# Optimization experiments

Measured on AMD Instinct MI355X. Metric: run time of the kernel, lower is better.

Reference implementation:

```python
import jax, jax.numpy as jnp
import numpy as np
import math

H = 128
HEADS = 2
NEG = -float(1 << 32)
BN_EPS = 1e-5
LN_EPS = 1e-5


def _bn_eval(x, g, b):
    # BatchNorm1d in eval mode with running_mean=0, running_var=1
    return g * (x / jnp.sqrt(1.0 + BN_EPS)) + b


def _ln(x, g, b):
    mu = x.mean(-1, keepdims=True)
    var = ((x - mu) ** 2).mean(-1, keepdims=True)
    return g * (x - mu) / jnp.sqrt(var + LN_EPS) + b


def _multi_embed(tables, idx):
    # tables [F,V,H], idx [N,F] -> sum_f tables[f, idx[:,f]]  (ogb Atom/BondEncoder)
    F = tables.shape[0]
    return tables[jnp.arange(F)[None, :], idx].sum(axis=1)


def _gin_graph(x, edge_attr, edge_index, batch, num_graphs, atom_emb, bond_emb, eps, w1, b1, g1, be1, w2, b2, g2, be2):
    h = _multi_embed(atom_emb, x)  # [N,H]
    tgt, src = edge_index[0], edge_index[1]
    L = eps.shape[0]
    for l in range(L):
        e = _multi_embed(bond_emb[l], edge_attr)  # [E,H]
        msg = jax.nn.relu(h[src] + e)
        agg = jax.ops.segment_sum(msg, tgt, num_segments=h.shape[0])
        z = (1.0 + eps[l]) * h + agg
        z = jax.nn.relu(_bn_eval(z @ w1[l] + b1[l], g1[l], be1[l])) @ w2[l] + b2[l]
        h = _bn_eval(z, g2[l], be2[l])
        if l != L - 1:
            h = jax.nn.relu(h)  # dropout is identity in eval mode
    s = jax.ops.segment_sum(h, batch, num_segments=num_graphs)
    c = jax.ops.segment_sum(jnp.ones_like(h), batch, num_segments=num_graphs)
    return s / (c + 1e-9)  # mean pooling per graph


def _sab(X, wq, bq, wk, bk, wv, bv, wo, bo, l1g, l1b, l2g, l2b):
    # MAB(X, X) with HEADS heads, use_ln=True. X: [B,S,H]
    B, S, _ = X.shape
    dh = H // HEADS

    def split(T):  # torch split(last)+cat(dim0): head-major [HEADS*B, S, dh]
        return T.reshape(B, S, HEADS, dh).transpose(2, 0, 1, 3).reshape(HEADS * B, S, dh)

    Qs, Ks, Vs = split(X @ wq + bq), split(X @ wk + bk), split(X @ wv + bv)
    A = jax.nn.softmax(jnp.einsum('bqd,bkd->bqk', Qs, Ks) / math.sqrt(dh), axis=-1)
    O = Qs + jnp.einsum('bqk,bkd->bqd', A, Vs)
    O = O.reshape(HEADS, B, S, dh).transpose(1, 2, 0, 3).reshape(B, S, H)
    O = _ln(O, l1g, l1b)
    O = _ln(O @ wo + bo, l2g, l2b)
    return O


def setup_inputs() -> dict:
    key = jax.random.key(0)
    ks = iter(jax.random.split(key, 64))
    nk = lambda: next(ks)
    V, L = 64, 4
    NS, ES = 60000, 140000
    NM, EM = 150000, 350000
    S, M, D, B = 492, 600, 200, 64
    f32 = jnp.float32
    w = lambda *shp: jax.random.normal(nk(), shp, f32) * 0.05
    inp = {}
    inp['atom_emb'] = w(2, 9, V, H)
    inp['bond_emb'] = w(2, L, 3, V, H)
    inp['gin_eps'] = jnp.zeros((2, L), f32)
    inp['gin_w1'] = w(2, L, H, 2 * H); inp['gin_b1'] = jnp.zeros((2, L, 2 * H), f32)
    inp['gin_bn1_g'] = jnp.ones((2, L, 2 * H), f32); inp['gin_bn1_b'] = jnp.zeros((2, L, 2 * H), f32)
    inp['gin_w2'] = w(2, L, 2 * H, H); inp['gin_b2'] = jnp.zeros((2, L, H), f32)
    inp['gin_bn2_g'] = jnp.ones((2, L, H), f32); inp['gin_bn2_b'] = jnp.zeros((2, L, H), f32)
    for nm in ['sab_wq', 'sab_wk', 'sab_wv', 'sab_wo']:
        inp[nm] = w(H, H)
    for nm in ['sab_bq', 'sab_bk', 'sab_bv', 'sab_bo', 'sab_ln1_b', 'sab_ln2_b']:
        inp[nm] = jnp.zeros((H,), f32)
    inp['sab_ln1_g'] = jnp.ones((H,), f32); inp['sab_ln2_g'] = jnp.ones((H,), f32)
    inp['agg_wq'] = w(H, H); inp['agg_bq'] = jnp.zeros((H,), f32)
    inp['agg_wk'] = w(H, H); inp['agg_bk'] = jnp.zeros((H,), f32)
    inp['score_w1'] = w(H, H // 2); inp['score_b1'] = jnp.zeros((H // 2,), f32)
    inp['score_w2'] = w(H // 2, 1); inp['score_b2'] = jnp.zeros((1,), f32)
    inp['patient_emb'] = jax.random.uniform(nk(), (B, S), f32)
    inp['average_projection'] = jax.random.uniform(nk(), (D, M), f32) / M
    inp['sub_x'] = jax.random.randint(nk(), (NS, 9), 0, V)
    inp['sub_edge_attr'] = jax.random.randint(nk(), (ES, 3), 0, V)
    inp['sub_edge_index'] = jax.random.randint(nk(), (2, ES), 0, NS)
    inp['sub_batch'] = jax.random.randint(nk(), (NS,), 0, S)
    inp['mol_x'] = jax.random.randint(nk(), (NM, 9), 0, V)
    inp['mol_edge_attr'] = jax.random.randint(nk(), (EM, 3), 0, V)
    inp['mol_edge_index'] = jax.random.randint(nk(), (2, EM), 0, NM)
    inp['mol_batch'] = jax.random.randint(nk(), (NM,), 0, M)
    mask = jax.random.bernoulli(nk(), 0.3, (D, S))
    inp['mask'] = mask.at[:, 0].set(False)
    inp['num_sub'] = S
    inp['num_mol'] = M
    return inp


def reference(atom_emb, bond_emb, gin_eps, gin_w1, gin_b1, gin_bn1_g, gin_bn1_b, gin_w2, gin_b2, gin_bn2_g, gin_bn2_b, sab_wq, sab_bq, sab_wk, sab_bk, sab_wv, sab_bv, sab_wo, sab_bo, sab_ln1_g, sab_ln1_b, sab_ln2_g, sab_ln2_b, agg_wq, agg_bq, agg_wk, agg_bk, score_w1, score_b1, score_w2, score_b2, patient_emb, average_projection, sub_x, sub_edge_attr, sub_edge_index, sub_batch, mol_x, mol_edge_attr, mol_edge_index, mol_batch, mask, num_sub, num_mol):
    # substructure encoder (GINGraph #0) + SAB interaction
    sub = _gin_graph(sub_x, sub_edge_attr, sub_edge_index, sub_batch, num_sub, atom_emb[0], bond_emb[0], gin_eps[0], gin_w1[0], gin_b1[0], gin_bn1_g[0], gin_bn1_b[0], gin_w2[0], gin_b2[0], gin_bn2_g[0], gin_bn2_b[0])
    sub = _sab(sub[None], sab_wq, sab_bq, sab_wk, sab_bk, sab_wv, sab_bv, sab_wo, sab_bo, sab_ln1_g, sab_ln1_b, sab_ln2_g, sab_ln2_b)[0]  # [S,H]
    # molecule encoder (GINGraph #1) + drug-level averaging
    mol = _gin_graph(mol_x, mol_edge_attr, mol_edge_index, mol_batch, num_mol, atom_emb[1], bond_emb[1], gin_eps[1], gin_w1[1], gin_b1[1], gin_bn1_g[1], gin_bn1_b[1], gin_w2[1], gin_b2[1], gin_bn2_g[1], gin_bn2_b[1])
    mol_emb = average_projection @ mol  # [D,H]
    # AttnAgg: masked attention, per-patient reweighting via diag(fix_feat)
    Q = mol_emb @ agg_wq + agg_bq
    K = sub @ agg_wk + agg_bk
    attn = (Q @ K.T) / math.sqrt(H)
    attn = jax.nn.softmax(jnp.where(mask, NEG, attn), axis=-1)  # [D,S]
    agg = jnp.einsum('ds,bs,sh->bdh', attn, patient_emb, sub)  # [B,D,H]
    logits = (jax.nn.relu(agg @ score_w1 + score_b1) @ score_w2 + score_b2)[..., 0]
    return jax.nn.sigmoid(logits)  # y_prob [B,D]
```

## Files before the change

### kernel.cpp

```cpp
#include <hip/hip_runtime.h>


typedef short short8 __attribute__((ext_vector_type(8)));
typedef unsigned short us8 __attribute__((ext_vector_type(8)));
typedef float f32x4 __attribute__((ext_vector_type(4)));
typedef unsigned short us4 __attribute__((ext_vector_type(4)));
typedef unsigned int u32;

#define BN_RSQ 0.9999950000374997f
#define LN_EPS 1e-5f
#define NEGBIG -4294967296.0f

__device__ __forceinline__ unsigned short f2bf(float x) {
  union { float f; unsigned int u; } v; v.f = x;
  unsigned int r = v.u + 0x7fffu + ((v.u >> 16) & 1u);
  return (unsigned short)(r >> 16);
}
__device__ __forceinline__ float bf2f(unsigned short x) {
  union { unsigned int u; float f; } v; v.u = ((unsigned int)x) << 16;
  return v.f;
}

__global__ __launch_bounds__(256) void prep_all(
    const float* __restrict__ w1, const float* __restrict__ w2,
    unsigned short* __restrict__ w1t, unsigned short* __restrict__ w2t,
    const float* __restrict__ bond, unsigned short* __restrict__ bt16, int bonde,
    const unsigned char* __restrict__ m, int* __restrict__ flags, int maskn) {
  __shared__ int lf[2];
  int b = blockIdx.x;
  if (b < 1024) {
    int i = b * 256 + threadIdx.x;
    int gl = i >> 15;
    int k1 = (i >> 8) & 127, c1 = i & 255;
    w1t[(gl << 15) + c1 * 128 + k1] = f2bf(w1[i]);
    int k2 = (i >> 7) & 255, c2 = i & 127;
    w2t[(gl << 15) + c2 * 256 + k2] = f2bf(w2[i]);
    return;
  }
  if (b < 1792) {
    int i = (b - 1024) * 256 + threadIdx.x;
    if (i < bonde) bt16[i] = f2bf(bond[i]);
    return;
  }
  if (threadIdx.x == 0) { lf[0] = 0; lf[1] = 0; }
  __syncthreads();
  int f0 = 0, f1 = 0;
  for (int i = (b - 1792) * 256 + threadIdx.x; i < maskn; i += 64 * 256) {
    if (m[i]) { if ((i & 3) == 0) f0 = 1; else f1 = 1; }
  }
  if (f0) atomicOr(&lf[0], 1);
  if (f1) atomicOr(&lf[1], 1);
  __syncthreads();
  if (threadIdx.x == 0) {
    if (lf[0]) atomicOr(flags, 1);
    if (lf[1]) atomicOr(flags + 1, 1);
  }
}

__global__ void build_count(const int* __restrict__ ei_m, int Em,
                            const int* __restrict__ ei_s, int Es,
                            const int* __restrict__ bm, int Nm,
                            const int* __restrict__ bs, int Ns,
                            int* __restrict__ deg_e, int* __restrict__ deg_n,
                            int M, int NmR) {
  int i = blockIdx.x * 256 + threadIdx.x;
  if (i < Em) { atomicAdd(&deg_e[ei_m[i]], 1); return; }
  i -= Em;
  if (i < Es) { atomicAdd(&deg_e[NmR + ei_s[i]], 1); return; }
  i -= Es;
  if (i < Nm) { atomicAdd(&deg_n[bm[i]], 1); return; }
  i -= Nm;
  if (i < Ns) { atomicAdd(&deg_n[M + bs[i]], 1); }
}

__global__ __launch_bounds__(256) void scan_block2(
    const int* __restrict__ cntE, int nE, int* __restrict__ exclE, int* __restrict__ bsumE, int nbE,
    const int* __restrict__ cntN, int nN, int* __restrict__ exclN, int* __restrict__ bsumN) {
  const int* cnt; int n; int* excl; int* bsum; int blk;
  if (blockIdx.x < (unsigned)nbE) { cnt = cntE; n = nE; excl = exclE; bsum = bsumE; blk = blockIdx.x; }
  else { cnt = cntN; n = nN; excl = exclN; bsum = bsumN; blk = blockIdx.x - nbE; }
  int gid = blk * 256 + threadIdx.x;
  int lane = threadIdx.x & 63, w = threadIdx.x >> 6;
  int v = (gid < n) ? cnt[gid] : 0;
  int x = v;
#pragma unroll
  for (int off = 1; off < 64; off <<= 1) {
    int y = __shfl_up(x, off, 64);
    if (lane >= off) x += y;
  }
  __shared__ int wt[4];
  if (lane == 63) wt[w] = x;
  __syncthreads();
  int add = 0;
  for (int i = 0; i < w; i++) add += wt[i];
  x += add;
  if (gid < n) excl[gid] = x - v;
  if (threadIdx.x == 255) bsum[blk] = x;
}

__global__ __launch_bounds__(1024) void scan_top2(int* __restrict__ bsumE, int nE,
                                                  int* __restrict__ bsumN, int nN) {
  int* bsum = blockIdx.x ? bsumN : bsumE;
  int n = blockIdx.x ? nN : nE;
  int t = threadIdx.x;
  int lane = t & 63, w = t >> 6;
  int v = (t < n) ? bsum[t] : 0;
  int x = v;
#pragma unroll
  for (int off = 1; off < 64; off <<= 1) {
    int y = __shfl_up(x, off, 64);
    if (lane >= off) x += y;
  }
  __shared__ int wt[16];
  if (lane == 63) wt[w] = x;
  __syncthreads();
  int add = 0;
  for (int i = 0; i < w; i++) add += wt[i];
  x += add;
  if (t < n) bsum[t] = x - v;
}

__global__ void finalize2(const int* __restrict__ exclE, const int* __restrict__ bsumE,
                          int nE, int totE, int* __restrict__ rowE,
                          const int* __restrict__ exclN, const int* __restrict__ bsumN,
                          int nN, int totN, int* __restrict__ rowN) {
  int i = blockIdx.x * 256 + threadIdx.x;
  if (i <= nE) {
    rowE[i] = (i < nE) ? (exclE[i] + bsumE[i >> 8]) : totE;
    return;
  }
  int j = i - nE - 1;
  if (j <= nN) rowN[j] = (j < nN) ? (exclN[j] + bsumN[j >> 8]) : totN;
}

__global__ void scatter2(const int* __restrict__ ei_m, const int* __restrict__ ea_m, int Em,
                         const int* __restrict__ ei_s, const int* __restrict__ ea_s, int Es, int NmR,
                         const int* __restrict__ rowptr_e, int* __restrict__ cur_e,
                         int4* __restrict__ epool,
                         const int* __restrict__ bm, int Nm,
                         const int* __restrict__ bs, int Ns, int M,
                         const int* __restrict__ rowptr_n, int* __restrict__ cur_n,
                         int* __restrict__ npool) {
  int i = blockIdx.x * 256 + threadIdx.x;
  if (i < Em + Es) {
    int g, src, a0, a1, a2;
    if (i < Em) {
      g = ei_m[i]; src = ei_m[Em + i];
      a0 = ea_m[i * 3]; a1 = ea_m[i * 3 + 1]; a2 = ea_m[i * 3 + 2];
    } else {
      int j = i - Em;
      g = NmR + ei_s[j]; src = NmR + ei_s[Es + j];
      a0 = ea_s[j * 3]; a1 = ea_s[j * 3 + 1]; a2 = ea_s[j * 3 + 2];
    }
    int slot = rowptr_e[g] + atomicAdd(&cur_e[g], 1);
    int p0 = a0 * 128, p1 = (64 + a1) * 128, p2 = (128 + a2) * 128;
    epool[slot] = make_int4(src * 128, 0, p0 | (p1 << 16), p2);
    return;
  }
  int k = i - (Em + Es);
  if (k >= Nm + Ns) return;
  int g, node;
  if (k < Nm) { g = bm[k]; node = k; }
  else { int j = k - Nm; g = M + bs[j]; node = NmR + j; }
  int slot = rowptr_n[g] + atomicAdd(&cur_n[g], 1);
  npool[slot] = node;
}

__global__ void embed2(const int* __restrict__ xm, const int* __restrict__ xs,
                       const float* __restrict__ atab, int Nm, int Ns, int NmR,
                       unsigned short* __restrict__ h) {
  int i = blockIdx.x * 256 + threadIdx.x;
  const int* x; const float* table; int n, c, outn;
  if (i < Nm * 128) {
    n = i >> 7; c = i & 127; x = xm; table = atab + (size_t)9 * 64 * 128; outn = n;
  } else {
    int j = i - Nm * 128;
    if (j >= Ns * 128) return;
    n = j >> 7; c = j & 127; x = xs; table = atab; outn = NmR + n;
  }
  float s = 0.f;
#pragma unroll
  for (int f = 0; f < 9; f++) {
    int v = x[n * 9 + f];
    s += table[(f * 64 + v) * 128 + c];
  }
  h[(size_t)outn * 128 + c] = f2bf(s);
}

__global__ __launch_bounds__(256, 4) void gin_fused3(
    const unsigned short* __restrict__ hin, unsigned short* __restrict__ hout,
    const float* __restrict__ eps_all, int l, int NmR,
    const unsigned short* __restrict__ bt16,
    const int4* __restrict__ epool, const int* __restrict__ rowptr_e,
    const unsigned short* __restrict__ w1t_a, const float* __restrict__ b1_a,
    const float* __restrict__ g1_a, const float* __restrict__ be1_a,
    const unsigned short* __restrict__ w2t_a, const float* __restrict__ b2_a,
    const float* __restrict__ g2_a, const float* __restrict__ be2_a) {
  __shared__ __align__(16) unsigned char smem[38144];
  unsigned short* z1s = (unsigned short*)smem;
  unsigned short* zs  = (unsigned short*)(smem + 20736);
  int t = threadIdx.x;
  int r0 = blockIdx.x * 64;
  int g = (r0 < NmR) ? 1 : 0;
  int gl = g * 4 + l;
  const unsigned short* bt = bt16 + (size_t)gl * 3 * 64 * 128;
  const unsigned short* w1t = w1t_a + (size_t)gl * 32768;
  const unsigned short* w2t = w2t_a + (size_t)gl * 32768;
  const float* b1 = b1_a + gl * 256;
  const float* g1 = g1_a + gl * 256;
  const float* be1 = be1_a + gl * 256;
  const float* b2 = b2_a + gl * 128;
  const float* g2 = g2_a + gl * 128;
  const float* be2 = be2_a + gl * 128;
  float eps1 = 1.0f + eps_all[gl];
  int do_relu = (l != 3);

#pragma unroll
  for (int p = 0; p < 2; p++) {
    int lr = p * 32 + (t >> 3);
    int n = r0 + lr;
    int cb = (t & 7) * 16;
    float lo[8], hi[8];
    {
      const u32* hr = (const u32*)(hin + (size_t)n * 128 + cb);
      uint4 h0v = *(const uint4*)hr;
      uint4 h1v = *(const uint4*)(hr + 4);
      u32 hd[8] = {h0v.x, h0v.y, h0v.z, h0v.w, h1v.x, h1v.y, h1v.z, h1v.w};
#pragma unroll
      for (int j = 0; j < 8; j++) {
        lo[j] = eps1 * __uint_as_float(hd[j] << 16);
        hi[j] = eps1 * __uint_as_float(hd[j] & 0xffff0000u);
      }
    }
    int e0 = rowptr_e[n], e1 = rowptr_e[n + 1];
    for (int e = e0; e < e1; e++) {
      int4 rec = epool[e];
      const u32* hs = (const u32*)(hin + rec.x + cb);
      const u32* q0 = (const u32*)(bt + (rec.z & 0xffff) + cb);
      const u32* q1 = (const u32*)(bt + (((unsigned)rec.z) >> 16) + cb);
      const u32* q2 = (const u32*)(bt + rec.w + cb);
      uint4 A0 = *(const uint4*)hs, A1 = *(const uint4*)(hs + 4);
      uint4 B0 = *(const uint4*)q0, B1 = *(const uint4*)(q0 + 4);
      uint4 C0 = *(const uint4*)q1, C1 = *(const uint4*)(q1 + 4);
      uint4 D0 = *(const uint4*)q2, D1 = *(const uint4*)(q2 + 4);
      u32 ad[8] = {A0.x, A0.y, A0.z, A0.w, A1.x, A1.y, A1.z, A1.w};
      u32 bd[8] = {B0.x, B0.y, B0.z, B0.w, B1.x, B1.y, B1.z, B1.w};
      u32 cd[8] = {C0.x, C0.y, C0.z, C0.w, C1.x, C1.y, C1.z, C1.w};
      u32 dd[8] = {D0.x, D0.y, D0.z, D0.w, D1.x, D1.y, D1.z, D1.w};
#pragma unroll
      for (int j = 0; j < 8; j++) {
        float sl = __uint_as_float(ad[j] << 16) + __uint_as_float(bd[j] << 16)
                 + __uint_as_float(cd[j] << 16) + __uint_as_float(dd[j] << 16);
        float sh = __uint_as_float(ad[j] & 0xffff0000u) + __uint_as_float(bd[j] & 0xffff0000u)
                 + __uint_as_float(cd[j] & 0xffff0000u) + __uint_as_float(dd[j] & 0xffff0000u);
        lo[j] += fmaxf(sl, 0.f);
        hi[j] += fmaxf(sh, 0.f);
      }
    }
    u32 od[8];
#pragma unroll
    for (int j = 0; j < 8; j++)
      od[j] = (u32)f2bf(lo[j]) | (((u32)f2bf(hi[j])) << 16);
    u32* zr = (u32*)(zs + lr * 136 + cb);
    *(uint4*)zr = make_uint4(od[0], od[1], od[2], od[3]);
    *(uint4*)(zr + 4) = make_uint4(od[4], od[5], od[6], od[7]);
  }
  __syncthreads();

  int lane = t & 63, wave = t >> 6;
  int quad = lane >> 4, l16 = lane & 15;
  {
    short8 bw[4][4];
    int cb = wave * 64;
#pragma unroll
    for (int nt = 0; nt < 4; nt++) {
      const unsigned short* p = w1t + (cb + nt * 16 + l16) * 128 + quad * 8;
#pragma unroll
      for (int kc = 0; kc < 4; kc++) bw[nt][kc] = *(const short8*)(p + kc * 32);
    }
    for (int mt = 0; mt < 4; mt++) {
      short8 af[4];
      const unsigned short* zrow = zs + (mt * 16 + l16) * 136 + quad * 8;
#pragma unroll
      for (int kc = 0; kc < 4; kc++)
        af[kc] = *(const short8*)(zrow + kc * 32);
#pragma unroll
      for (int nt = 0; nt < 4; nt++) {
        f32x4 acc = {0.f, 0.f, 0.f, 0.f};
#pragma unroll
        for (int kc = 0; kc < 4; kc++)
          acc = __builtin_amdgcn_mfma_f32_16x16x32_bf16(af[kc], bw[nt][kc], acc, 0, 0, 0);
        int c = cb + nt * 16 + l16;
        float sc = g1[c] * BN_RSQ, sh = be1[c], bb = b1[c];
#pragma unroll
        for (int reg = 0; reg < 4; reg++) {
          int r = mt * 16 + quad * 4 + reg;
          float y = (acc[reg] + bb) * sc + sh;
          z1s[r * 264 + c] = f2bf(fmaxf(y, 0.f));
        }
      }
      __syncthreads();
    }
  }
  {
    short8 bw[2][8];
    int cb = wave * 32;
#pragma unroll
    for (int nt = 0; nt < 2; nt++) {
      const unsigned short* p = w2t + (cb + nt * 16 + l16) * 256 + quad * 8;
#pragma unroll
      for (int kc = 0; kc < 8; kc++) bw[nt][kc] = *(const short8*)(p + kc * 32);
    }
    for (int mt = 0; mt < 4; mt++) {
      short8 af[8];
      const unsigned short* zrow = z1s + (mt * 16 + l16) * 264 + quad * 8;
#pragma unroll
      for (int kc = 0; kc < 8; kc++)
        af[kc] = *(const short8*)(zrow + kc * 32);
      __syncthreads();
#pragma unroll
      for (int nt = 0; nt < 2; nt++) {
        f32x4 acc = {0.f, 0.f, 0.f, 0.f};
#pragma unroll
        for (int kc = 0; kc < 8; kc++)
          acc = __builtin_amdgcn_mfma_f32_16x16x32_bf16(af[kc], bw[nt][kc], acc, 0, 0, 0);
        int c = cb + nt * 16 + l16;
        float sc = g2[c] * BN_RSQ, sh = be2[c], bb = b2[c];
#pragma unroll
        for (int reg = 0; reg < 4; reg++) {
          int r = mt * 16 + quad * 4 + reg;
          float y = (acc[reg] + bb) * sc + sh;
          if (do_relu) y = fmaxf(y, 0.f);
          z1s[r * 264 + c] = f2bf(y);
        }
      }
    }
  }
  __syncthreads();
  for (int i = t; i < 1024; i += 256) {
    int r = i >> 4, c8 = (i & 15) * 8;
    us8 v = *(const us8*)(z1s + r * 264 + c8);
    *(us8*)(hout + (size_t)(r0 + r) * 128 + c8) = v;
  }
}

__global__ __launch_bounds__(128) void pool_csr(const unsigned short* __restrict__ h,
                                                const int* __restrict__ npool,
                                                const int* __restrict__ rowptr_n,
                                                float* __restrict__ pooled, int nseg) {
  int m = blockIdx.x;
  if (m >= nseg) return;
  int st = rowptr_n[m];
  int e = rowptr_n[m + 1];
  int len = e - st;
  int c = threadIdx.x;
  float s = 0.f;
  int i = st;
  for (; i + 3 < e; i += 4) {
    int n0 = npool[i], n1 = npool[i + 1], n2 = npool[i + 2], n3 = npool[i + 3];
    float v0 = bf2f(h[(size_t)n0 * 128 + c]);
    float v1 = bf2f(h[(size_t)n1 * 128 + c]);
    float v2 = bf2f(h[(size_t)n2 * 128 + c]);
    float v3 = bf2f(h[(size_t)n3 * 128 + c]);
    s += (v0 + v1) + (v2 + v3);
  }
  for (; i < e; i++) s += bf2f(h[(size_t)npool[i] * 128 + c]);
  pooled[m * 128 + c] = s / ((float)len + 1e-9f);
}

__global__ __launch_bounds__(256) void gemm_tile(const float* __restrict__ A, const float* __restrict__ W,
                                                 const float* __restrict__ bias, float* __restrict__ C,
                                                 int K) {
  __shared__ float As[608];
  __shared__ float red[128];
  int r = blockIdx.x;
  int t = threadIdx.x;
  for (int i = t; i < K; i += 256) As[i] = A[(size_t)r * K + i];
  __syncthreads();
  int c = t & 127, half = t >> 7;
  int Kh = K >> 1;
  int k0 = half * Kh, k1 = k0 + Kh;
  float acc = 0.f;
#pragma unroll 8
  for (int k = k0; k < k1; k++) acc = fmaf(As[k], W[(size_t)k * 128 + c], acc);
  if (half) red[c] = acc;
  __syncthreads();
  if (!half) {
    float v = acc + red[c] + (bias ? bias[c] : 0.f);
    C[(size_t)r * 128 + c] = v;
  }
}

__global__ __launch_bounds__(256) void gemm_qkv(const float* __restrict__ A,
                                                const float* __restrict__ W0, const float* __restrict__ bi0, float* __restrict__ C0,
                                                const float* __restrict__ W1, const float* __restrict__ bi1, float* __restrict__ C1,
                                                const float* __restrict__ W2, const float* __restrict__ bi2, float* __restrict__ C2) {
  __shared__ float As[128];
  __shared__ float red[128];
  int r = blockIdx.x, which = blockIdx.y;
  const float* W = (which == 0) ? W0 : (which == 1) ? W1 : W2;
  const float* bias = (which == 0) ? bi0 : (which == 1) ? bi1 : bi2;
  float* C = (which == 0) ? C0 : (which == 1) ? C1 : C2;
  int t = threadIdx.x;
  if (t < 128) As[t] = A[(size_t)r * 128 + t];
  __syncthreads();
  int c = t & 127, half = t >> 7;
  int k0 = half * 64, k1 = k0 + 64;
  float acc = 0.f;
#pragma unroll 8
  for (int k = k0; k < k1; k++) acc = fmaf(As[k], W[(size_t)k * 128 + c], acc);
  if (half) red[c] = acc;
  __syncthreads();
  if (!half) C[(size_t)r * 128 + c] = acc + red[c] + bias[c];
}

__global__ __launch_bounds__(256) void gemm_aggqk(
    const float* __restrict__ Aq, const float* __restrict__ Wq, const float* __restrict__ bq,
    float* __restrict__ Cq, int D,
    const float* __restrict__ Ak, const float* __restrict__ Wk, const float* __restrict__ bk,
    float* __restrict__ Ck) {
  __shared__ float As[128];
  __shared__ float red[128];
  int r = blockIdx.x;
  const float* A; const float* W; const float* bias; float* C; int rr;
  if (r < D) { A = Aq; W = Wq; bias = bq; C = Cq; rr = r; }
  else { A = Ak; W = Wk; bias = bk; C = Ck; rr = r - D; }
  int t = threadIdx.x;
  if (t < 128) As[t] = A[(size_t)rr * 128 + t];
  __syncthreads();
  int c = t & 127, half = t >> 7;
  int k0 = half * 64, k1 = k0 + 64;
  float acc = 0.f;
#pragma unroll 8
  for (int k = k0; k < k1; k++) acc = fmaf(As[k], W[(size_t)k * 128 + c], acc);
  if (half) red[c] = acc;
  __syncthreads();
  if (!half) C[(size_t)rr * 128 + c] = acc + red[c] + bias[c];
}

__global__ __launch_bounds__(256) void gemm_wo_ln(const float* __restrict__ A,
                                                  const float* __restrict__ W, const float* __restrict__ bias,
                                                  const float* __restrict__ lg, const float* __restrict__ lb,
                                                  float* __restrict__ subf) {
  __shared__ float As[128];
  __shared__ float row[128];
  __shared__ float red2[4];
  int r = blockIdx.x;
  int t = threadIdx.x;
  if (t < 128) As[t] = A[(size_t)r * 128 + t];
  __syncthreads();
  int c = t & 127, half = t >> 7;
  int k0 = half * 64, k1 = k0 + 64;
  float acc = 0.f;
#pragma unroll 8
  for (int k = k0; k < k1; k++) acc = fmaf(As[k], W[(size_t)k * 128 + c], acc);
  if (half) row[c] = acc;
  __syncthreads();
  if (!half) row[c] = acc + row[c] + bias[c];
  __syncthreads();
  if (t < 128) {
    float x = row[t];
    float s = x;
    for (int off = 32; off; off >>= 1) s += __shfl_down(s, off);
    if ((t & 63) == 0) red2[t >> 6] = s;
  }
  __syncthreads();
  if (t < 128) {
    float mu = (red2[0] + red2[1]) * (1.f / 128.f);
    float dd = row[t] - mu;
    float v = dd * dd;
    for (int off = 32; off; off >>= 1) v += __shfl_down(v, off);
    if ((t & 63) == 0) red2[2 + (t >> 6)] = v;
  }
  __syncthreads();
  if (t < 128) {
    float mu = (red2[0] + red2[1]) * (1.f / 128.f);
    float var = (red2[2] + red2[3]) * (1.f / 128.f);
    float dd = row[t] - mu;
    subf[(size_t)r * 128 + t] = lg[t] * dd * rsqrtf(var + LN_EPS) + lb[t];
  }
}

__global__ __launch_bounds__(256) void sab_attn(const float* __restrict__ Q, const float* __restrict__ K,
                                                const float* __restrict__ V, float* __restrict__ O, int S) {
  int q = blockIdx.x, hd = blockIdx.y;
  int t = threadIdx.x;
  __shared__ float sc[512];
  __shared__ float red[8];
  __shared__ float pacc[4][64];
  const float* qrow = Q + q * 128 + hd * 64;
  for (int k = t; k < 512; k += 256) {
    float d = -1e30f;
    if (k < S) {
      const float* krow = K + k * 128 + hd * 64;
      d = 0.f;
#pragma unroll
      for (int j = 0; j < 64; j += 4) {
        float4 a = *(const float4*)(qrow + j);
        float4 b = *(const float4*)(krow + j);
        d += a.x * b.x + a.y * b.y + a.z * b.z + a.w * b.w;
      }
      d *= 0.125f;
    }
    sc[k] = d;
  }
  __syncthreads();
  float m = fmaxf(sc[t], sc[t + 256]);
  for (int off = 32; off; off >>= 1) m = fmaxf(m, __shfl_down(m, off));
  if ((t & 63) == 0) red[t >> 6] = m;
  __syncthreads();
  m = fmaxf(fmaxf(red[0], red[1]), fmaxf(red[2], red[3]));
  float p0 = __expf(sc[t] - m), p1 = __expf(sc[t + 256] - m);
  sc[t] = p0; sc[t + 256] = p1;
  float s = p0 + p1;
  for (int off = 32; off; off >>= 1) s += __shfl_down(s, off);
  if ((t & 63) == 0) red[4 + (t >> 6)] = s;
  __syncthreads();
  float inv = 1.f / (red[4] + red[5] + red[6] + red[7]);
  int d = t & 63, part = t >> 6;
  float acc = 0.f;
  for (int k = part; k < S; k += 4) acc += sc[k] * V[k * 128 + hd * 64 + d];
  pacc[part][d] = acc;
  __syncthreads();
  if (part == 0) {
    float o = (pacc[0][d] + pacc[1][d] + pacc[2][d] + pacc[3][d]) * inv;
    O[q * 128 + hd * 64 + d] = qrow[d] + o;
  }
}

__global__ __launch_bounds__(128) void ln_rows(const float* __restrict__ in, float* __restrict__ out,
                                               const float* __restrict__ g, const float* __restrict__ b) {
  int r = blockIdx.x, t = threadIdx.x;
  __shared__ float red[4];
  float x = in[r * 128 + t];
  float s = x;
  for (int off = 32; off; off >>= 1) s += __shfl_down(s, off);
  if ((t & 63) == 0) red[t >> 6] = s;
  __syncthreads();
  float mu = (red[0] + red[1]) * (1.f / 128.f);
  float dd = x - mu;
  float v = dd * dd;
  for (int off = 32; off; off >>= 1) v += __shfl_down(v, off);
  if ((t & 63) == 0) red[2 + (t >> 6)] = v;
  __syncthreads();
  float var = (red[2] + red[3]) * (1.f / 128.f);
  out[r * 128 + t] = g[t] * dd * rsqrtf(var + LN_EPS) + b[t];
}

__global__ __launch_bounds__(256) void agg_attn(const float* __restrict__ Q, const float* __restrict__ Kt,
                                                const void* __restrict__ mask, const int* __restrict__ flags,
                                                float* __restrict__ attn, int D, int S) {
  int d = blockIdx.x, t = threadIdx.x;
  __shared__ float sc[512];
  __shared__ float red[8];
  int layout = (flags[1] == 0) ? 0 : (flags[0] ? 1 : 2);
  const float* qrow = Q + d * 128;
  for (int s = t; s < 512; s += 256) {
    float v = NEGBIG;
    if (s < S) {
      int mi = d * S + s;
      bool msk;
      if (layout == 0)      msk = ((const int*)mask)[mi] != 0;
      else if (layout == 1) msk = ((const unsigned char*)mask)[mi] != 0;
      else                  msk = ((const float*)mask)[mi] != 0.f;
      if (!msk) {
        float dd = 0.f;
        const float* krow = Kt + s * 128;
#pragma unroll
        for (int j = 0; j < 128; j += 4) {
          float4 a = *(const float4*)(qrow + j);
          float4 b = *(const float4*)(krow + j);
          dd += a.x * b.x + a.y * b.y + a.z * b.z + a.w * b.w;
        }
        v = dd * 0.08838834764831845f;
      }
    }
    sc[s] = v;
  }
  __syncthreads();
  float m = fmaxf(sc[t], sc[t + 256]);
  for (int off = 32; off; off >>= 1) m = fmaxf(m, __shfl_down(m, off));
  if ((t & 63) == 0) red[t >> 6] = m;
  __syncthreads();
  m = fmaxf(fmaxf(red[0], red[1]), fmaxf(red[2], red[3]));
  float p0 = __expf(sc[t] - m), p1 = __expf(sc[t + 256] - m);
  float s2 = p0 + p1;
  for (int off = 32; off; off >>= 1) s2 += __shfl_down(s2, off);
  if ((t & 63) == 0) red[4 + (t >> 6)] = s2;
  __syncthreads();
  float inv = 1.f / (red[4] + red[5] + red[6] + red[7]);
  attn[d * S + t] = p0 * inv;
  if (t + 256 < S) attn[d * S + t + 256] = p1 * inv;
}

__global__ void prep_subT(const float* __restrict__ subf, unsigned short* __restrict__ subT, int S) {
  int i = blockIdx.x * 256 + threadIdx.x;
  if (i >= 128 * 512) return;
  int hh = i >> 9, k = i & 511;
  subT[i] = (k < S) ? f2bf(subf[k * 128 + hh]) : (unsigned short)0;
}

__global__ __launch_bounds__(256) void agg_mfma(const float* __restrict__ attn, const float* __restrict__ pat,
                                                const unsigned short* __restrict__ subT,
                                                float* __restrict__ aggT, int D, int S) {
  int d = blockIdx.x, t = threadIdx.x;
  __shared__ unsigned short As[64][40];
  int lane = t & 63, wave = t >> 6;
  int quad = lane >> 4, l16 = lane & 15;
  f32x4 acc[8];
#pragma unroll
  for (int nt = 0; nt < 8; nt++) acc[nt] = (f32x4){0.f, 0.f, 0.f, 0.f};
  const float* arow = attn + d * S;
  int srow = t >> 2, skb = (t & 3) * 8;
  for (int c = 0; c < 16; c++) {
    int s0 = c * 32;
    __syncthreads();
    unsigned short v[8];
#pragma unroll
    for (int j = 0; j < 8; j++) {
      int s = s0 + skb + j;
      float x = (s < S) ? arow[s] * pat[srow * S + s] : 0.f;
      v[j] = f2bf(x);
    }
    *(us4*)&As[srow][skb]     = *(us4*)&v[0];
    *(us4*)&As[srow][skb + 4] = *(us4*)&v[4];
    __syncthreads();
    short8 af = *(const short8*)&As[16 * wave + l16][quad * 8];
#pragma unroll
    for (int nt = 0; nt < 8; nt++) {
      short8 bf = *(const short8*)(subT + (nt * 16 + l16) * 512 + s0 + quad * 8);
      acc[nt] = __builtin_amdgcn_mfma_f32_16x16x32_bf16(af, bf, acc[nt], 0, 0, 0);
    }
  }
#pragma unroll
  for (int nt = 0; nt < 8; nt++) {
    int hh = nt * 16 + l16;
#pragma unroll
    for (int reg = 0; reg < 4; reg++) {
      int b = 16 * wave + quad * 4 + reg;
      aggT[((size_t)(b * D + d)) * 128 + hh] = acc[nt][reg];
    }
  }
}

__global__ __launch_bounds__(256) void score_head(const float* __restrict__ aggT,
                                                  const float* __restrict__ w1, const float* __restrict__ b1,
                                                  const float* __restrict__ w2, const float* __restrict__ b2,
                                                  float* __restrict__ out, int total) {
  int i = blockIdx.x * 4 + (threadIdx.x >> 6);
  int j = threadIdx.x & 63;
  if (i >= total) return;
  const float* av = aggT + (size_t)i * 128;
  float acc = b1[j];
#pragma unroll 8
  for (int k = 0; k < 128; k++) acc = fmaf(av[k], w1[k * 64 + j], acc);
  acc = fmaxf(acc, 0.f) * w2[j];
  for (int off = 32; off; off >>= 1) acc += __shfl_down(acc, off);
  if (j == 0) {
    float x = acc + b2[0];
    out[i] = 1.f / (1.f + __expf(-x));
  }
}

extern "C" void kernel_launch(void* const* d_in, const int* in_sizes, int n_in,
                              void* d_out, int out_size, void* d_ws, size_t ws_size,
                              hipStream_t stream) {
  const float* atom_emb = (const float*)d_in[0];
  const float* bond_emb = (const float*)d_in[1];
  const float* gin_eps  = (const float*)d_in[2];
  const float* gin_w1   = (const float*)d_in[3];
  const float* gin_b1   = (const float*)d_in[4];
  const float* bn1g     = (const float*)d_in[5];
  const float* bn1b     = (const float*)d_in[6];
  const float* gin_w2   = (const float*)d_in[7];
  const float* gin_b2   = (const float*)d_in[8];
  const float* bn2g     = (const float*)d_in[9];
  const float* bn2b     = (const float*)d_in[10];
  const float* sab_wq = (const float*)d_in[11];
  const float* sab_wk = (const float*)d_in[12];
  const float* sab_wv = (const float*)d_in[13];
  const float* sab_wo = (const float*)d_in[14];
  const float* sab_bq = (const float*)d_in[15];
  const float* sab_bk = (const float*)d_in[16];
  const float* sab_bv = (const float*)d_in[17];
  const float* sab_bo = (const float*)d_in[18];
  const float* ln1b = (const float*)d_in[19];
  const float* ln2b = (const float*)d_in[20];
  const float* ln1g = (const float*)d_in[21];
  const float* ln2g = (const float*)d_in[22];
  const float* agg_wq = (const float*)d_in[23];
  const float* agg_bq = (const float*)d_in[24];
  const float* agg_wk = (const float*)d_in[25];
  const float* agg_bk = (const float*)d_in[26];
  const float* score_w1 = (const float*)d_in[27];
  const float* score_b1 = (const float*)d_in[28];
  const float* score_w2 = (const float*)d_in[29];
  const float* score_b2 = (const float*)d_in[30];
  const float* patient  = (const float*)d_in[31];
  const float* avgproj  = (const float*)d_in[32];
  const int* sub_x     = (const int*)d_in[33];
  const int* sub_ea    = (const int*)d_in[34];
  const int* sub_ei    = (const int*)d_in[35];
  const int* sub_batch = (const int*)d_in[36];
  const int* mol_x     = (const int*)d_in[37];
  const int* mol_ea    = (const int*)d_in[38];
  const int* mol_ei    = (const int*)d_in[39];
  const int* mol_batch = (const int*)d_in[40];
  const void* mask     = d_in[41];

  const int Ns = in_sizes[33] / 9, Es = in_sizes[34] / 3;
  const int Nm = in_sizes[37] / 9, Em = in_sizes[38] / 3;
  const int S = 492, M = 600, D = 200, B = 64;
  const int NmR = (Nm + 63) & ~63;
  const int NsR = (Ns + 63) & ~63;
  const int NTOT = NmR + NsR;
  const int NSEG = M + S;
  const int ETOT = Em + Es;
  const int BONDE = 2 * 4 * 3 * 64 * 128;

  char* Wp = (char*)d_ws;
  size_t off = 0;
  auto alloc = [&](size_t bytes) -> void* {
    void* p = Wp + off;
    off = (off + bytes + 255) & ~(size_t)255;
    return p;
  };
  unsigned short* h0 = (unsigned short*)alloc((size_t)NTOT * 128 * 2);
  unsigned short* h1 = (unsigned short*)alloc((size_t)NTOT * 128 * 2);
  unsigned short* w1t = (unsigned short*)alloc(262144 * 2);
  unsigned short* w2t = (unsigned short*)alloc(262144 * 2);
  unsigned short* bt16 = (unsigned short*)alloc((size_t)BONDE * 2);
  int4* epool  = (int4*)alloc((size_t)ETOT * 16);
  int*  npool  = (int*)alloc((size_t)(Nm + Ns) * 4);
  int*  excl_e = (int*)alloc((size_t)NTOT * 4);
  int*  bsum_e = (int*)alloc(1024 * 4);
  int*  excl_n = (int*)alloc((size_t)NSEG * 4);
  int*  bsum_n = (int*)alloc(1024 * 4);
  int*  rowptr_e = (int*)alloc((size_t)(NTOT + 1) * 4);
  int*  rowptr_n = (int*)alloc((size_t)(NSEG + 1) * 4);
  char* zstart = Wp + off;
  int*  deg_e  = (int*)alloc((size_t)NTOT * 4);
  int*  deg_n  = (int*)alloc((size_t)NSEG * 4);
  int*  cur_e  = (int*)alloc((size_t)NTOT * 4);
  int*  cur_n  = (int*)alloc((size_t)NSEG * 4);
  int*  flags  = (int*)alloc(8);
  size_t zsize = (size_t)((Wp + off) - zstart);
  float* pooled_all = (float*)alloc((size_t)NSEG * 128 * 4);
  float* pooled_mol = pooled_all;
  float* pooled_sub = pooled_all + (size_t)M * 128;
  float* Qb   = (float*)alloc((size_t)S * 128 * 4);
  float* Kb   = (float*)alloc((size_t)S * 128 * 4);
  float* Vb   = (float*)alloc((size_t)S * 128 * 4);
  float* Ob   = (float*)alloc((size_t)S * 128 * 4);
  float* subf = (float*)alloc((size_t)S * 128 * 4);
  unsigned short* subT = (unsigned short*)alloc((size_t)128 * 512 * 2);
  float* mol_embb = (float*)alloc((size_t)D * 128 * 4);
  float* aggQb = (float*)alloc((size_t)D * 128 * 4);
  float* aggKb = (float*)alloc((size_t)S * 128 * 4);
  float* attnb = (float*)alloc((size_t)D * S * 4);
  float* aggTb = (float*)alloc((size_t)B * D * 128 * 4);
  (void)ws_size; (void)n_in; (void)out_size;

  hipMemsetAsync(zstart, 0, zsize, stream);
  prep_all<<<1856, 256, 0, stream>>>(gin_w1, gin_w2, w1t, w2t,
                                     bond_emb, bt16, BONDE,
                                     (const unsigned char*)mask, flags, D * S);

  int total_cnt = Em + Es + Nm + Ns;
  build_count<<<(total_cnt + 255) / 256, 256, 0, stream>>>(
      mol_ei, Em, sub_ei, Es, mol_batch, Nm, sub_batch, Ns, deg_e, deg_n, M, NmR);
  int nb_e = (NTOT + 255) / 256;
  int nb_n = (NSEG + 255) / 256;
  scan_block2<<<nb_e + nb_n, 256, 0, stream>>>(deg_e, NTOT, excl_e, bsum_e, nb_e,
                                               deg_n, NSEG, excl_n, bsum_n);
  scan_top2<<<2, 1024, 0, stream>>>(bsum_e, nb_e, bsum_n, nb_n);
  finalize2<<<((NTOT + 1) + (NSEG + 1) + 1 + 255) / 256, 256, 0, stream>>>(
      excl_e, bsum_e, NTOT, ETOT, rowptr_e,
      excl_n, bsum_n, NSEG, Nm + Ns, rowptr_n);
  scatter2<<<(ETOT + Nm + Ns + 255) / 256, 256, 0, stream>>>(
      mol_ei, mol_ea, Em, sub_ei, sub_ea, Es, NmR, rowptr_e, cur_e, epool,
      mol_batch, Nm, sub_batch, Ns, M, rowptr_n, cur_n, npool);

  embed2<<<((Nm + Ns) * 128 + 255) / 256, 256, 0, stream>>>(
      mol_x, sub_x, atom_emb, Nm, Ns, NmR, h0);
  unsigned short* hin = h0; unsigned short* hout = h1;
  for (int l = 0; l < 4; l++) {
    gin_fused3<<<NTOT / 64, 256, 0, stream>>>(
        hin, hout, gin_eps, l, NmR, bt16, epool, rowptr_e,
        w1t, gin_b1, bn1g, bn1b, w2t, gin_b2, bn2g, bn2b);
    unsigned short* tmp = hin; hin = hout; hout = tmp;
  }
  pool_csr<<<NSEG, 128, 0, stream>>>(hin, npool, rowptr_n, pooled_all, NSEG);

  gemm_qkv<<<dim3(S, 3), 256, 0, stream>>>(pooled_sub,
                                           sab_wq, sab_bq, Qb,
                                           sab_wk, sab_bk, Kb,
                                           sab_wv, sab_bv, Vb);
  sab_attn<<<dim3(S, 2), 256, 0, stream>>>(Qb, Kb, Vb, Ob, S);
  ln_rows<<<S, 128, 0, stream>>>(Ob, Ob, ln1g, ln1b);
  gemm_wo_ln<<<S, 256, 0, stream>>>(Ob, sab_wo, sab_bo, ln2g, ln2b, subf);
  prep_subT<<<(128 * 512 + 255) / 256, 256, 0, stream>>>(subf, subT, S);

  gemm_tile<<<D, 256, 0, stream>>>(avgproj, pooled_mol, (const float*)nullptr, mol_embb, 600);

  gemm_aggqk<<<D + S, 256, 0, stream>>>(mol_embb, agg_wq, agg_bq, aggQb, D,
                                        subf, agg_wk, agg_bk, aggKb);
  agg_attn<<<D, 256, 0, stream>>>(aggQb, aggKb, mask, flags, attnb, D, S);
  agg_mfma<<<D, 256, 0, stream>>>(attnb, patient, subT, aggTb, D, S);
  score_head<<<(B * D + 3) / 4, 256, 0, stream>>>(aggTb, score_w1, score_b1, score_w2, score_b2,
                                                  (float*)d_out, B * D);
}
```

Measured before the change: 1.016 ms.

## Compact edge records, stage them in LDS per block, vectorize atom embedding

Shrinks each CSR edge record from 16 to 8 bytes by packing the three bond attribute indices into one 18-bit field and computing table offsets in the kernel. Each GIN block now cooperatively loads its contiguous range of edge records into shared memory (up to a cap, with global fallback beyond it) before the per-node aggregation loop. This replaces the per-thread redundant global reads, since eight threads share each node's records. The atom embedding kernel is also vectorized to four channels per thread with float4 loads and packed bf16 stores. The shared buffer aliases the z1s region, so correctness depends on a barrier before the later writes to z1s.

```diff
diff --git a/kernel.cpp b/kernel.cpp
--- a/kernel.cpp
+++ b/kernel.cpp
@@ -136,7 +136,7 @@
 __global__ void scatter2(const int* __restrict__ ei_m, const int* __restrict__ ea_m, int Em,
                          const int* __restrict__ ei_s, const int* __restrict__ ea_s, int Es, int NmR,
                          const int* __restrict__ rowptr_e, int* __restrict__ cur_e,
-                         int4* __restrict__ epool,
+                         int2* __restrict__ epool,
                          const int* __restrict__ bm, int Nm,
                          const int* __restrict__ bs, int Ns, int M,
                          const int* __restrict__ rowptr_n, int* __restrict__ cur_n,
@@ -153,8 +153,7 @@
       a0 = ea_s[j * 3]; a1 = ea_s[j * 3 + 1]; a2 = ea_s[j * 3 + 2];
     }
     int slot = rowptr_e[g] + atomicAdd(&cur_e[g], 1);
-    int p0 = a0 * 128, p1 = (64 + a1) * 128, p2 = (128 + a2) * 128;
-    epool[slot] = make_int4(src * 128, 0, p0 | (p1 << 16), p2);
+    epool[slot] = make_int2(src * 128, a0 | (a1 << 6) | (a2 << 12));
     return;
   }
   int k = i - (Em + Es);
@@ -170,28 +169,31 @@
                        const float* __restrict__ atab, int Nm, int Ns, int NmR,
                        unsigned short* __restrict__ h) {
   int i = blockIdx.x * 256 + threadIdx.x;
-  const int* x; const float* table; int n, c, outn;
-  if (i < Nm * 128) {
-    n = i >> 7; c = i & 127; x = xm; table = atab + (size_t)9 * 64 * 128; outn = n;
+  const int* x; const float* table; int n, cq, outn;
+  if (i < Nm * 32) {
+    n = i >> 5; cq = (i & 31) * 4; x = xm; table = atab + (size_t)9 * 64 * 128; outn = n;
   } else {
-    int j = i - Nm * 128;
-    if (j >= Ns * 128) return;
-    n = j >> 7; c = j & 127; x = xs; table = atab; outn = NmR + n;
-  }
-  float s = 0.f;
+    int j = i - Nm * 32;
+    if (j >= Ns * 32) return;
+    n = j >> 5; cq = (j & 31) * 4; x = xs; table = atab; outn = NmR + n;
+  }
+  float4 s = make_float4(0.f, 0.f, 0.f, 0.f);
 #pragma unroll
   for (int f = 0; f < 9; f++) {
     int v = x[n * 9 + f];
-    s += table[(f * 64 + v) * 128 + c];
-  }
-  h[(size_t)outn * 128 + c] = f2bf(s);
+    float4 tv = *(const float4*)(table + (size_t)(f * 64 + v) * 128 + cq);
+    s.x += tv.x; s.y += tv.y; s.z += tv.z; s.w += tv.w;
+  }
+  us4 o;
+  o.x = f2bf(s.x); o.y = f2bf(s.y); o.z = f2bf(s.z); o.w = f2bf(s.w);
+  *(us4*)(h + (size_t)outn * 128 + cq) = o;
 }
 
 __global__ __launch_bounds__(256, 4) void gin_fused3(
     const unsigned short* __restrict__ hin, unsigned short* __restrict__ hout,
     const float* __restrict__ eps_all, int l, int NmR,
     const unsigned short* __restrict__ bt16,
-    const int4* __restrict__ epool, const int* __restrict__ rowptr_e,
+    const int2* __restrict__ epool, const int* __restrict__ rowptr_e,
     const unsigned short* __restrict__ w1t_a, const float* __restrict__ b1_a,
     const float* __restrict__ g1_a, const float* __restrict__ be1_a,
     const unsigned short* __restrict__ w2t_a, const float* __restrict__ b2_a,
@@ -199,6 +201,8 @@
   __shared__ __align__(16) unsigned char smem[38144];
   unsigned short* z1s = (unsigned short*)smem;
   unsigned short* zs  = (unsigned short*)(smem + 20736);
+  int2* recs = (int2*)smem;
+  const int CAP = 2592;
   int t = threadIdx.x;
   int r0 = blockIdx.x * 64;
   int g = (r0 < NmR) ? 1 : 0;
@@ -215,6 +219,12 @@
   float eps1 = 1.0f + eps_all[gl];
   int do_relu = (l != 3);
 
+  int e0 = rowptr_e[r0], e1 = rowptr_e[r0 + 64];
+  int nE = e1 - e0;
+  int nstage = (nE < CAP) ? nE : CAP;
+  for (int i = t; i < nstage; i += 256) recs[i] = epool[e0 + i];
+  __syncthreads();
+
 #pragma unroll
   for (int p = 0; p < 2; p++) {
     int lr = p * 32 + (t >> 3);
@@ -232,13 +242,14 @@
         hi[j] = eps1 * __uint_as_float(hd[j] & 0xffff0000u);
       }
     }
-    int e0 = rowptr_e[n], e1 = rowptr_e[n + 1];
-    for (int e = e0; e < e1; e++) {
-      int4 rec = epool[e];
+    int le0 = rowptr_e[n] - e0, le1 = rowptr_e[n + 1] - e0;
+    for (int li = le0; li < le1; li++) {
+      int2 rec = (li < CAP) ? recs[li] : epool[e0 + li];
+      u32 ab = (u32)rec.y;
       const u32* hs = (const u32*)(hin + rec.x + cb);
-      const u32* q0 = (const u32*)(bt + (rec.z & 0xffff) + cb);
-      const u32* q1 = (const u32*)(bt + (((unsigned)rec.z) >> 16) + cb);
-      const u32* q2 = (const u32*)(bt + rec.w + cb);
+      const u32* q0 = (const u32*)(bt + (ab & 63u) * 128 + cb);
+      const u32* q1 = (const u32*)(bt + (64 + ((ab >> 6) & 63u)) * 128 + cb);
+      const u32* q2 = (const u32*)(bt + (128 + ((ab >> 12) & 63u)) * 128 + cb);
       uint4 A0 = *(const uint4*)hs, A1 = *(const uint4*)(hs + 4);
       uint4 B0 = *(const uint4*)q0, B1 = *(const uint4*)(q0 + 4);
       uint4 C0 = *(const uint4*)q1, C1 = *(const uint4*)(q1 + 4);
@@ -730,7 +741,7 @@
   unsigned short* w1t = (unsigned short*)alloc(262144 * 2);
   unsigned short* w2t = (unsigned short*)alloc(262144 * 2);
   unsigned short* bt16 = (unsigned short*)alloc((size_t)BONDE * 2);
-  int4* epool  = (int4*)alloc((size_t)ETOT * 16);
+  int2* epool  = (int2*)alloc((size_t)ETOT * 8);
   int*  npool  = (int*)alloc((size_t)(Nm + Ns) * 4);
   int*  excl_e = (int*)alloc((size_t)NTOT * 4);
   int*  bsum_e = (int*)alloc(1024 * 4);
@@ -781,7 +792,7 @@
       mol_ei, mol_ea, Em, sub_ei, sub_ea, Es, NmR, rowptr_e, cur_e, epool,
       mol_batch, Nm, sub_batch, Ns, M, rowptr_n, cur_n, npool);
 
-  embed2<<<((Nm + Ns) * 128 + 255) / 256, 256, 0, stream>>>(
+  embed2<<<((Nm + Ns) * 32 + 255) / 256, 256, 0, stream>>>(
       mol_x, sub_x, atom_emb, Nm, Ns, NmR, h0);
   unsigned short* hin = h0; unsigned short* hout = h1;
   for (int l = 0; l < 4; l++) {
```

Measured after the change: 963.5 us. 5.1% less time.
